# Kernel tuning notes

Hardware: AMD Instinct MI355X
Metric: run time of the kernel (lower is better)

Reference implementation:

```python
import jax, jax.numpy as jnp
import numpy as np
from jax import lax

EPS = 1e-5  # nn.BatchNorm2d default eps


def _binarize_act(x):
    # out = sign(x).detach() - clip(x).detach() + clip(x)  (STE)
    c = jnp.clip(x, -1.0, 1.0)
    return c + lax.stop_gradient(jnp.sign(x) - c)


def _binarize_weight(w):
    # w.data = w.fp.sign().add(0.01).sign()  -> {-1,+1}, zeros map to +1.
    # Autograd in torch sees identity wrt the parameter (data swap), i.e. STE.
    wb = jnp.sign(jnp.sign(w) + 0.01)
    return w + lax.stop_gradient(wb - w)


def setup_inputs() -> dict:
    key = jax.random.key(0)
    k1, k2, k3, k4 = jax.random.split(key, 4)
    N, Cin, Cout, H, W = 16, 32, 32, 256, 256
    return {
        "x": jax.random.normal(k1, (N, Cin, H, W), dtype=jnp.float32),
        "weight": jax.random.normal(k2, (Cout, Cin, 3, 3), dtype=jnp.float32),
        "gamma": jnp.ones((Cout,), dtype=jnp.float32),
        "beta": jnp.zeros((Cout,), dtype=jnp.float32),
        "running_mean": jax.random.normal(k3, (Cout,), dtype=jnp.float32) * 0.1,
        "running_var": jax.random.uniform(k4, (Cout,), dtype=jnp.float32) + 0.5,
    }


def reference(x, weight, gamma, beta, running_mean, running_var):
    xb = _binarize_act(x)
    wb = _binarize_weight(weight)
    # 3x3, stride 1, padding 1 -> SAME spatial size
    out = lax.conv_general_dilated(
        xb, wb,
        window_strides=(1, 1),
        padding=((1, 1), (1, 1)),
        dimension_numbers=("NCHW", "OIHW", "NCHW"),
    )
    # BatchNorm2d (inference form with running stats), then ReLU
    inv = gamma / jnp.sqrt(running_var + EPS)  # [C]
    out = out * inv[None, :, None, None] + (beta - running_mean * inv)[None, :, None, None]
    return jax.nn.relu(out)
```

## Files before the change

kernel.cpp:

```cpp
#include <hip/hip_runtime.h>
#include <stdint.h>

#define NB   16
#define CIN  32
#define COUT 32
#define HH   256
#define WW   256
#define HWSZ (HH * WW)
#define EPSV 1e-5f

typedef int v4i  __attribute__((ext_vector_type(4)));
typedef int v16i __attribute__((ext_vector_type(16)));

__global__ __launch_bounds__(288) void pack_w_kernel(
    const float* __restrict__ wt, const float* __restrict__ gamma,
    const float* __restrict__ beta, const float* __restrict__ rmean,
    const float* __restrict__ rvar, uint4* __restrict__ afrag,
    float* __restrict__ c0f, float* __restrict__ c1f) {
    __shared__ uint32_t pws[COUT * 9];
    const int j = threadIdx.x;
    if (j < COUT * 9) {
        const int o = j / 9, t = j % 9;
        uint32_t bits = 0;
#pragma unroll
        for (int c = 0; c < CIN; ++c)
            bits |= (wt[(o * CIN + c) * 9 + t] < 0.f) ? (1u << c) : 0u;
        pws[j] = bits;
    }
    __syncthreads();
    if (j < 64) {
        const int sh = (j & 32) >> 1;
#pragma unroll
        for (int t = 0; t < 9; ++t) {
            const uint32_t chunk = pws[(j & 31) * 9 + t] >> sh;
            uint32_t w[4];
#pragma unroll
            for (int k = 0; k < 4; ++k) {
                const uint32_t y = (((chunk >> (4 * k)) & 0xFu) * 0x204081u) & 0x01010101u;
                w[k] = (y * 0xFEu) | 0x01010101u;
            }
            afrag[t * 64 + j] = make_uint4(w[0], w[1], w[2], w[3]);
        }
    }
    {
        const int cls = j >> 5;
        const int o   = j & 31;
        const int rc = cls / 3, cc = cls % 3;
        int wsum = 0;
#pragma unroll
        for (int dh = 0; dh < 3; ++dh)
#pragma unroll
            for (int dw = 0; dw < 3; ++dw) {
                const bool bad = (rc == 0 && dh == 0) || (rc == 2 && dh == 2) ||
                                 (cc == 0 && dw == 0) || (cc == 2 && dw == 2);
                if (!bad) wsum += 32 - 2 * __popc(pws[o * 9 + dh * 3 + dw]);
            }
        const float inv = gamma[o] * rsqrtf(rvar[o] + EPSV);
        c0f[cls * 32 + o] = beta[o] - rmean[o] * inv - (float)wsum * inv;
        if (cls == 0) c1f[o] = 2.0f * inv;
    }
}

__global__ __launch_bounds__(256) void biconv_mfma(
    const uint32_t* __restrict__ x, const uint4* __restrict__ afrag,
    const float* __restrict__ c0f, const float* __restrict__ c1f,
    float* __restrict__ out) {
    const uint32_t bid = blockIdx.x;
    const uint32_t wg  = ((bid & 7u) << 8) | (bid >> 3);
    const int n   = wg >> 7;
    const int h0  = (wg & 127) << 1;
    const int tid  = threadIdx.x;
    const int lane = tid & 63;
    const int wave = tid >> 6;

    __shared__ uint32_t tiles[4 * 264];
    __shared__ float    c0sh[9 * COUT];
    __shared__ float    c1sh[COUT];

    for (int i = tid; i < 9 * COUT; i += 256) c0sh[i] = c0f[i];
    if (tid < COUT) c1sh[tid] = c1f[tid];
    if (tid < 8) tiles[(tid >> 1) * 264 + ((tid & 1) ? 260 : 3)] = 0u;

    {
        const int r = wave, q = tid & 63;
        const int hr = h0 - 1 + r;
        uint32_t b0 = 0, b1 = 0, b2 = 0, b3 = 0;
        if (hr >= 0 && hr < HH) {
            const uint32_t* xp = x + (size_t)n * (CIN * HWSZ) + hr * WW + (q << 2);
#pragma unroll
            for (int c = 0; c < CIN; ++c) {
                const uint4 v = *reinterpret_cast<const uint4*>(xp + (size_t)c * HWSZ);
                b0 |= (v.x >> 31) << c;
                b1 |= (v.y >> 31) << c;
                b2 |= (v.z >> 31) << c;
                b3 |= (v.w >> 31) << c;
            }
            b0 = ~b0; b1 = ~b1; b2 = ~b2; b3 = ~b3;
        }
        *reinterpret_cast<uint4*>(&tiles[r * 264 + (q << 2) + 4]) =
            make_uint4(b0, b1, b2, b3);
    }
    __syncthreads();

    v4i af[9];
#pragma unroll
    for (int t = 0; t < 9; ++t)
        af[t] = *reinterpret_cast<const v4i*>(&afrag[t * 64 + lane]);
    const int shv = (lane & 32) >> 1;
    const int og  = (lane >> 5) << 2;

#pragma unroll
    for (int r = 0; r < 2; ++r) {
        const int h  = h0 + r;
        const int rc = (h == 0) ? 0 : ((h == HH - 1) ? 2 : 1);
#pragma unroll
        for (int tw = 0; tw < 2; ++tw) {
            const int w0    = (wave << 6) + (tw << 5);
            const int pixel = w0 + (lane & 31);
            const uint32_t* bp = &tiles[r * 264 + pixel + 3];
            v16i acc = {0};
#pragma unroll
            for (int dh = 0; dh < 3; ++dh) {
#pragma unroll
                for (int dw = 0; dw < 3; ++dw) {
                    const uint32_t h16 = bp[dh * 264 + dw] >> shv;
                    v4i b;
                    b.x = (int)(((( h16        ) & 0xFu) * 0x204081u) & 0x01010101u);
                    b.y = (int)((((h16 >> 4   ) & 0xFu) * 0x204081u) & 0x01010101u);
                    b.z = (int)((((h16 >> 8   ) & 0xFu) * 0x204081u) & 0x01010101u);
                    b.w = (int)((((h16 >> 12  ) & 0xFu) * 0x204081u) & 0x01010101u);
                    acc = __builtin_amdgcn_mfma_i32_32x32x32_i8(af[dh * 3 + dw], b,
                                                                acc, 0, 0, 0);
                }
            }
            const int ccls = (pixel == 0) ? 0 : ((pixel == WW - 1) ? 2 : 1);
            const float* c0b = &c0sh[(rc * 3 + ccls) * 32];
            float* outp = out + (size_t)n * (COUT * HWSZ) + (size_t)h * WW + pixel;
#pragma unroll
            for (int e = 0; e < 16; ++e) {
                const int o = (e & 3) + ((e >> 2) << 3) + og;
                const float v = fmaf((float)acc[e], c1sh[o], c0b[o]);
                __builtin_nontemporal_store(v > 0.f ? v : 0.f,
                                            outp + (size_t)o * HWSZ);
            }
        }
    }
}

extern "C" void kernel_launch(void* const* d_in, const int* in_sizes, int n_in,
                              void* d_out, int out_size, void* d_ws, size_t ws_size,
                              hipStream_t stream) {
    const float* x     = (const float*)d_in[0];
    const float* wt    = (const float*)d_in[1];
    const float* gamma = (const float*)d_in[2];
    const float* beta  = (const float*)d_in[3];
    const float* rmean = (const float*)d_in[4];
    const float* rvar  = (const float*)d_in[5];
    float* out = (float*)d_out;

    uint4* afrag = (uint4*)d_ws;
    float* c0f   = (float*)((char*)d_ws + 9216);
    float* c1f   = c0f + 288;

    pack_w_kernel<<<dim3(1), dim3(288), 0, stream>>>(wt, gamma, beta, rmean,
                                                     rvar, afrag, c0f, c1f);
    biconv_mfma<<<dim3(NB * HH / 2), dim3(256), 0, stream>>>(
        (const uint32_t*)x, afrag, c0f, c1f, out);
}
```

Before: 54.69 us.

## Process one output row per block with shared weight fragments and dual accumulators

Each block now computes a single output row instead of two, loading 3 input rows instead of 4, and the grid doubles. Weight fragments move from per-lane registers into shared memory, loaded by the spare fourth wave while the other three pack input bits. Each wave now runs two independent MFMA accumulator chains over adjacent 32-pixel tiles that share each A fragment, and launch bounds request 6 blocks per SIMD for occupancy. The trade-off is more redundant input reads per output row (3 rows per output row instead of 2), in exchange for fewer registers, more interleaved MFMA chains and higher occupancy.

```diff
diff --git a/kernel.cpp b/kernel.cpp
--- a/kernel.cpp
+++ b/kernel.cpp
@@ -8,6 +8,7 @@
 #define WW   256
 #define HWSZ (HH * WW)
 #define EPSV 1e-5f
+#define TWD  264
 
 typedef int v4i  __attribute__((ext_vector_type(4)));
 typedef int v16i __attribute__((ext_vector_type(16)));
@@ -16,7 +17,7 @@
     const float* __restrict__ wt, const float* __restrict__ gamma,
     const float* __restrict__ beta, const float* __restrict__ rmean,
     const float* __restrict__ rvar, uint4* __restrict__ afrag,
-    float* __restrict__ c0f, float* __restrict__ c1f) {
+    float* __restrict__ c0f) {
     __shared__ uint32_t pws[COUT * 9];
     const int j = threadIdx.x;
     if (j < COUT * 9) {
@@ -57,36 +58,32 @@
             }
         const float inv = gamma[o] * rsqrtf(rvar[o] + EPSV);
         c0f[cls * 32 + o] = beta[o] - rmean[o] * inv - (float)wsum * inv;
-        if (cls == 0) c1f[o] = 2.0f * inv;
+        if (cls == 0) c0f[288 + o] = 2.0f * inv;
     }
 }
 
-__global__ __launch_bounds__(256) void biconv_mfma(
+__global__ __launch_bounds__(256, 6) void biconv_mfma(
     const uint32_t* __restrict__ x, const uint4* __restrict__ afrag,
-    const float* __restrict__ c0f, const float* __restrict__ c1f,
-    float* __restrict__ out) {
+    const float* __restrict__ c0f, float* __restrict__ out) {
     const uint32_t bid = blockIdx.x;
-    const uint32_t wg  = ((bid & 7u) << 8) | (bid >> 3);
-    const int n   = wg >> 7;
-    const int h0  = (wg & 127) << 1;
+    const uint32_t wg  = ((bid & 7u) << 9) | (bid >> 3);
+    const int n   = wg >> 8;
+    const int h   = wg & 255;
     const int tid  = threadIdx.x;
     const int lane = tid & 63;
     const int wave = tid >> 6;
 
-    __shared__ uint32_t tiles[4 * 264];
-    __shared__ float    c0sh[9 * COUT];
-    __shared__ float    c1sh[COUT];
+    __shared__ uint32_t tiles[3][TWD];
+    __shared__ uint4    afsh[9 * 64];
+    __shared__ float    csh[320];
 
-    for (int i = tid; i < 9 * COUT; i += 256) c0sh[i] = c0f[i];
-    if (tid < COUT) c1sh[tid] = c1f[tid];
-    if (tid < 8) tiles[(tid >> 1) * 264 + ((tid & 1) ? 260 : 3)] = 0u;
-
-    {
-        const int r = wave, q = tid & 63;
-        const int hr = h0 - 1 + r;
+    if (tid < 192) {
+        const int r  = tid >> 6;
+        const int q  = tid & 63;
+        const int hr = h - 1 + r;
         uint32_t b0 = 0, b1 = 0, b2 = 0, b3 = 0;
         if (hr >= 0 && hr < HH) {
-            const uint32_t* xp = x + (size_t)n * (CIN * HWSZ) + hr * WW + (q << 2);
+            const uint32_t* xp = x + (size_t)n * (CIN * HWSZ) + (size_t)hr * WW + (q << 2);
 #pragma unroll
             for (int c = 0; c < CIN; ++c) {
                 const uint4 v = *reinterpret_cast<const uint4*>(xp + (size_t)c * HWSZ);
@@ -97,53 +94,60 @@
             }
             b0 = ~b0; b1 = ~b1; b2 = ~b2; b3 = ~b3;
         }
-        *reinterpret_cast<uint4*>(&tiles[r * 264 + (q << 2) + 4]) =
-            make_uint4(b0, b1, b2, b3);
+        *reinterpret_cast<uint4*>(&tiles[r][(q << 2) + 4]) = make_uint4(b0, b1, b2, b3);
+    } else {
+        const int t2 = tid - 192;
+#pragma unroll
+        for (int k = 0; k < 9; ++k) afsh[t2 + 64 * k] = afrag[t2 + 64 * k];
+#pragma unroll
+        for (int k = 0; k < 5; ++k) csh[t2 + 64 * k] = c0f[t2 + 64 * k];
+        if (t2 < 6) tiles[t2 >> 1][(t2 & 1) ? 260 : 3] = 0u;
     }
     __syncthreads();
 
-    v4i af[9];
-#pragma unroll
-    for (int t = 0; t < 9; ++t)
-        af[t] = *reinterpret_cast<const v4i*>(&afrag[t * 64 + lane]);
+    const int l31 = lane & 31;
     const int shv = (lane & 32) >> 1;
     const int og  = (lane >> 5) << 2;
+    const int pA  = (wave << 6) + l31;
+    const int pB  = pA + 32;
 
+    v16i acc0 = {0}, acc1 = {0};
 #pragma unroll
-    for (int r = 0; r < 2; ++r) {
-        const int h  = h0 + r;
-        const int rc = (h == 0) ? 0 : ((h == HH - 1) ? 2 : 1);
+    for (int dh = 0; dh < 3; ++dh) {
+        const uint32_t* trow = &tiles[dh][0];
 #pragma unroll
-        for (int tw = 0; tw < 2; ++tw) {
-            const int w0    = (wave << 6) + (tw << 5);
-            const int pixel = w0 + (lane & 31);
-            const uint32_t* bp = &tiles[r * 264 + pixel + 3];
-            v16i acc = {0};
+        for (int dw = 0; dw < 3; ++dw) {
+            const v4i a = *reinterpret_cast<const v4i*>(&afsh[(dh * 3 + dw) * 64 + lane]);
+            const uint32_t hA = trow[pA + 3 + dw] >> shv;
+            const uint32_t hB = trow[pB + 3 + dw] >> shv;
+            v4i b;
+            b.x = (int)((( hA        & 0xFu) * 0x204081u) & 0x01010101u);
+            b.y = (int)((((hA >> 4)  & 0xFu) * 0x204081u) & 0x01010101u);
+            b.z = (int)((((hA >> 8)  & 0xFu) * 0x204081u) & 0x01010101u);
+            b.w = (int)((((hA >> 12) & 0xFu) * 0x204081u) & 0x01010101u);
+            acc0 = __builtin_amdgcn_mfma_i32_32x32x32_i8(a, b, acc0, 0, 0, 0);
+            b.x = (int)((( hB        & 0xFu) * 0x204081u) & 0x01010101u);
+            b.y = (int)((((hB >> 4)  & 0xFu) * 0x204081u) & 0x01010101u);
+            b.z = (int)((((hB >> 8)  & 0xFu) * 0x204081u) & 0x01010101u);
+            b.w = (int)((((hB >> 12) & 0xFu) * 0x204081u) & 0x01010101u);
+            acc1 = __builtin_amdgcn_mfma_i32_32x32x32_i8(a, b, acc1, 0, 0, 0);
+        }
+    }
+
+    const int rc   = (h == 0) ? 0 : ((h == HH - 1) ? 2 : 1);
+    const int ccA  = (pA == 0) ? 0 : ((pA == WW - 1) ? 2 : 1);
+    const int ccB  = (pB == WW - 1) ? 2 : 1;
+    const float* c0A = &csh[(rc * 3 + ccA) * 32];
+    const float* c0B = &csh[(rc * 3 + ccB) * 32];
+    const float* c1  = &csh[288];
+    float* outp = out + (size_t)n * (COUT * HWSZ) + (size_t)h * WW;
 #pragma unroll
-            for (int dh = 0; dh < 3; ++dh) {
-#pragma unroll
-                for (int dw = 0; dw < 3; ++dw) {
-                    const uint32_t h16 = bp[dh * 264 + dw] >> shv;
-                    v4i b;
-                    b.x = (int)(((( h16        ) & 0xFu) * 0x204081u) & 0x01010101u);
-                    b.y = (int)((((h16 >> 4   ) & 0xFu) * 0x204081u) & 0x01010101u);
-                    b.z = (int)((((h16 >> 8   ) & 0xFu) * 0x204081u) & 0x01010101u);
-                    b.w = (int)((((h16 >> 12  ) & 0xFu) * 0x204081u) & 0x01010101u);
-                    acc = __builtin_amdgcn_mfma_i32_32x32x32_i8(af[dh * 3 + dw], b,
-                                                                acc, 0, 0, 0);
-                }
-            }
-            const int ccls = (pixel == 0) ? 0 : ((pixel == WW - 1) ? 2 : 1);
-            const float* c0b = &c0sh[(rc * 3 + ccls) * 32];
-            float* outp = out + (size_t)n * (COUT * HWSZ) + (size_t)h * WW + pixel;
-#pragma unroll
-            for (int e = 0; e < 16; ++e) {
-                const int o = (e & 3) + ((e >> 2) << 3) + og;
-                const float v = fmaf((float)acc[e], c1sh[o], c0b[o]);
-                __builtin_nontemporal_store(v > 0.f ? v : 0.f,
-                                            outp + (size_t)o * HWSZ);
-            }
-        }
+    for (int e = 0; e < 16; ++e) {
+        const int o = (e & 3) + ((e >> 2) << 3) + og;
+        const float vA = fmaf((float)acc0[e], c1[o], c0A[o]);
+        const float vB = fmaf((float)acc1[e], c1[o], c0B[o]);
+        __builtin_nontemporal_store(vA > 0.f ? vA : 0.f, outp + (size_t)o * HWSZ + pA);
+        __builtin_nontemporal_store(vB > 0.f ? vB : 0.f, outp + (size_t)o * HWSZ + pB);
     }
 }
 
@@ -160,10 +164,9 @@
 
     uint4* afrag = (uint4*)d_ws;
     float* c0f   = (float*)((char*)d_ws + 9216);
-    float* c1f   = c0f + 288;
 
     pack_w_kernel<<<dim3(1), dim3(288), 0, stream>>>(wt, gamma, beta, rmean,
-                                                     rvar, afrag, c0f, c1f);
-    biconv_mfma<<<dim3(NB * HH / 2), dim3(256), 0, stream>>>(
-        (const uint32_t*)x, afrag, c0f, c1f, out);
+                                                     rvar, afrag, c0f);
+    biconv_mfma<<<dim3(NB * HH), dim3(256), 0, stream>>>(
+        (const uint32_t*)x, afrag, c0f, out);
 }
```

Result: faster. 50.42 us (-7.8%).
